# Performance work log

Hardware: AMD Instinct MI355X
Metric: run time of the kernel (lower is better)

## Reference

```python
import jax, jax.numpy as jnp
import numpy as np

B, N, C, H, REG = 1, 2309, 1024, 16, 5
D = C // H


def setup_inputs() -> dict:
    key = jax.random.key(0)
    k0, k1, k2, k3 = jax.random.split(key, 4)
    x = jax.random.normal(k0, (B, N, C), dtype=jnp.float32)
    g_info = jax.random.normal(k1, (12, 2, C), dtype=jnp.float32)
    W_qkv = jax.random.normal(k2, (C, 3 * C), dtype=jnp.float32) * 0.02
    W_proj = jax.random.normal(k3, (C, C), dtype=jnp.float32) * 0.02
    b_proj = jnp.zeros((C,), dtype=jnp.float32)
    return {"x": x, "g_info": g_info, "W_qkv": W_qkv, "W_proj": W_proj, "b_proj": b_proj}


def reference(x, g_info, W_qkv, W_proj, b_proj):
    Bx, Nx, Cx = x.shape
    scale = D ** -0.5
    # qkv projection (qkv_bias=False)
    qkv = (x @ W_qkv).reshape(Bx, Nx, 3, H, D)
    q, k, v = qkv[:, :, 0], qkv[:, :, 1], qkv[:, :, 2]  # [B,N,H,D]

    # grounding query vector from layer 0
    g_layer = g_info[0].reshape(-1, H, D)
    q_g = g_layer[0]  # [H,D]

    # cosine-similarity routing over non-register tokens
    q_pure = q[:, REG:]  # [B,M,H,D]
    q_n = q_pure / jnp.linalg.norm(q_pure, axis=-1, keepdims=True)
    qg_n = q_g / jnp.linalg.norm(q_g, axis=-1, keepdims=True)
    sim = (qg_n[None, None] * q_n).sum(-1).mean(-1)  # [B,M]
    sim = (sim - sim.min()) / (sim.max() - sim.min())  # global min-max normalize
    pos = sim > 0.9  # [B,M] boolean routing mask

    # Full logits computed once; group attention = masked softmax over the
    # group's key set (registers always included). This is mathematically
    # identical to the torch gather->attend->scatter, with static shapes.
    logits = jnp.einsum('bqhd,bkhd->bhqk', q * scale, k)  # [B,H,N,N]

    def masked_attn(tok_mask):
        key_mask = jnp.concatenate([jnp.ones((Bx, REG), bool), tok_mask], axis=1)  # [B,N]
        l = jnp.where(key_mask[:, None, None, :], logits, -jnp.inf)
        a = jax.nn.softmax(l, axis=-1)
        return jnp.einsum('bhqk,bkhd->bqhd', a, v)  # [B,N,H,D]

    x_pos = masked_attn(pos)
    x_neg = masked_attn(~pos)

    reg_out = (x_pos[:, :REG] + x_neg[:, :REG]) * 0.5
    tok_out = jnp.where(pos[:, :, None, None], x_pos[:, REG:], x_neg[:, REG:])
    out = jnp.concatenate([reg_out, tok_out], axis=1).reshape(Bx, Nx, Cx)
    return out @ W_proj + b_proj
```

## Files before the change

### kernel.cpp

```cpp
#include <hip/hip_runtime.h>
#include <math.h>

#define TOK 2309
#define CH 1024
#define NH 16
#define HD 64
#define NREG 5
#define NTOK (TOK - NREG)
#define NPADQ 2432
#define NPAD2 2560
#define NKT 40
#define HTILES 20
#define NQROW 2368
#define QSCL 0.1803368801f

typedef unsigned short ushort_t;
typedef unsigned char uchar_t;
typedef __attribute__((ext_vector_type(8))) short s8frag;
typedef __attribute__((ext_vector_type(4))) float f4frag;
typedef __attribute__((ext_vector_type(2))) long ll2;

__device__ __forceinline__ float wredsum(float v){
  #pragma unroll
  for (int o = 32; o > 0; o >>= 1) v += __shfl_xor(v, o, 64);
  return v;
}

__device__ __forceinline__ unsigned short f2bf(float x){
  union { float f; unsigned u; } v; v.f = x;
  unsigned r = v.u + 0x7FFF + ((v.u >> 16) & 1);
  return (unsigned short)(r >> 16);
}
__device__ __forceinline__ float bf2f(unsigned short u){
  union { unsigned u32; float f; } v; v.u32 = ((unsigned)u) << 16;
  return v.f;
}
__device__ __forceinline__ unsigned pack_bf16(float lo, float hi){
  union { float f; unsigned u; } a, b;
  a.f = lo; b.f = hi;
  return __builtin_amdgcn_perm(b.u + 0x8000u, a.u + 0x8000u, 0x07060302u);
}
__device__ __forceinline__ uchar_t f2fp8(float x){
  return (uchar_t)(__builtin_amdgcn_cvt_pk_fp8_f32(x, x, 0, false) & 0xff);
}
__device__ __forceinline__ void cp16(const void* g, void* l){
  __builtin_amdgcn_global_load_lds(
      (const __attribute__((address_space(1))) unsigned int*)g,
      (__attribute__((address_space(3))) unsigned int*)l, 16, 0, 0);
}

__global__ __launch_bounds__(256) void split_x_kernel(
    const float* __restrict__ X, ushort_t* __restrict__ Xhi, ushort_t* __restrict__ Xlo)
{
  int row = blockIdx.x;
  int c4 = threadIdx.x * 4;
  ushort4 h4 = {0,0,0,0}, l4 = {0,0,0,0};
  if (row < TOK) {
    float4 v = *(const float4*)&X[(size_t)row*CH + c4];
    float vv[4] = {v.x, v.y, v.z, v.w};
    ushort_t hs[4], ls[4];
    #pragma unroll
    for (int i = 0; i < 4; i++) {
      hs[i] = f2bf(vv[i]);
      ls[i] = f2bf(vv[i] - bf2f(hs[i]));
    }
    h4.x=hs[0]; h4.y=hs[1]; h4.z=hs[2]; h4.w=hs[3];
    l4.x=ls[0]; l4.y=ls[1]; l4.z=ls[2]; l4.w=ls[3];
  }
  *(ushort4*)&Xhi[(size_t)row*CH + c4] = h4;
  *(ushort4*)&Xlo[(size_t)row*CH + c4] = l4;
}

__global__ __launch_bounds__(256) void pack_w_kernel(
    const float* __restrict__ W, const int N,
    ushort_t* __restrict__ WT, ushort_t* __restrict__ WloT, const int loN)
{
  __shared__ float T[64][68];
  const int tid = threadIdx.x;
  const int n0 = blockIdx.x * 64;
  const int k0 = blockIdx.y * 64;
  const int lr = tid >> 4;
  const int lc = (tid & 15) * 4;
  #pragma unroll
  for (int s = 0; s < 4; s++) {
    float4 v = *(const float4*)&W[(size_t)(k0 + lr + s*16) * N + n0 + lc];
    *(float4*)&T[lr + s*16][lc] = v;
  }
  __syncthreads();
  const int nl = tid >> 2;
  const int kc = (tid & 3) * 16;
  const bool dolo = (WloT != nullptr) && (n0 < loN);
  ushort_t* dh = WT + (size_t)(n0 + nl) * CH + k0 + kc;
  ushort_t* dl = WloT + (size_t)(n0 + nl) * CH + k0 + kc;
  #pragma unroll
  for (int g = 0; g < 4; g++) {
    float a = T[kc+g*4+0][nl], b = T[kc+g*4+1][nl];
    float c = T[kc+g*4+2][nl], d = T[kc+g*4+3][nl];
    ushort4 oh;
    oh.x=f2bf(a); oh.y=f2bf(b); oh.z=f2bf(c); oh.w=f2bf(d);
    *(ushort4*)&dh[g*4] = oh;
    if (dolo) {
      ushort4 ol;
      ol.x=f2bf(a-bf2f(oh.x)); ol.y=f2bf(b-bf2f(oh.y));
      ol.z=f2bf(c-bf2f(oh.z)); ol.w=f2bf(d-bf2f(oh.w));
      *(ushort4*)&dl[g*4] = ol;
    }
  }
}

__global__ __launch_bounds__(256) void gemm_qkv_mfma(
    const ushort_t* __restrict__ Xhi, const ushort_t* __restrict__ Xlo,
    const ushort_t* __restrict__ WhiT, const ushort_t* __restrict__ WloT,
    float* __restrict__ Qf, uchar_t* __restrict__ Q8,
    uchar_t* __restrict__ K8, ushort_t* __restrict__ Vbf)
{
  __shared__ ushort_t LA[2][2][4096];
  __shared__ ushort_t LB[2][2][4096];
  const int tid = threadIdx.x;
  const int w = tid >> 6, lane = tid & 63;
  const int quad = lane >> 4, c16 = lane & 15;
  const int wm = w >> 1, wn = w & 1;
  const int nt = blockIdx.x, mt = blockIdx.y;
  const int n0 = nt * 128, m0 = mt * 128;
  const bool isQ = (nt < 8);

  const int srow = tid >> 2;
  const int g = (tid & 3) ^ ((tid >> 3) & 3);
  const size_t aoff = (size_t)(m0 + srow)*CH + g*8;
  const size_t boff = (size_t)(n0 + srow)*CH + g*8;
  const int lbase = (tid & 192) * 8;

  f4frag acc[4][4];
  #pragma unroll
  for (int mi = 0; mi < 4; mi++)
    #pragma unroll
    for (int nb = 0; nb < 4; nb++) acc[mi][nb] = (f4frag){0.f,0.f,0.f,0.f};

  const int soff = (quad ^ ((c16 >> 1) & 3)) * 8;
  int aro[4], bro[4];
  #pragma unroll
  for (int i = 0; i < 4; i++) {
    aro[i] = (wm*64 + i*16 + c16)*32 + soff;
    bro[i] = (wn*64 + i*16 + c16)*32 + soff;
  }

#define QKV_STAGE(KT, BUF) {                                                   \
    const int _k = (KT)*32;                                                    \
    cp16(Xhi  + aoff + _k,                 &LA[BUF][0][lbase]);                \
    cp16(Xhi  + aoff + _k + (size_t)64*CH, &LA[BUF][0][2048 + lbase]);         \
    cp16(WhiT + boff + _k,                 &LB[BUF][0][lbase]);                \
    cp16(WhiT + boff + _k + (size_t)64*CH, &LB[BUF][0][2048 + lbase]);         \
    if (isQ) {                                                                 \
      cp16(Xlo  + aoff + _k,                 &LA[BUF][1][lbase]);              \
      cp16(Xlo  + aoff + _k + (size_t)64*CH, &LA[BUF][1][2048 + lbase]);       \
      cp16(WloT + boff + _k,                 &LB[BUF][1][lbase]);              \
      cp16(WloT + boff + _k + (size_t)64*CH, &LB[BUF][1][2048 + lbase]);       \
    } }

  QKV_STAGE(0, 0);
  for (int kt = 0; kt < 32; kt++) {
    const int buf = kt & 1;
    __syncthreads();
    if (kt < 31) { QKV_STAGE(kt+1, buf^1); }
    s8frag a[4], b[4];
    #pragma unroll
    for (int i = 0; i < 4; i++) a[i] = *(const s8frag*)&LA[buf][0][aro[i]];
    #pragma unroll
    for (int i = 0; i < 4; i++) b[i] = *(const s8frag*)&LB[buf][0][bro[i]];
    #pragma unroll
    for (int mi = 0; mi < 4; mi++)
      #pragma unroll
      for (int nb = 0; nb < 4; nb++)
        acc[mi][nb] = __builtin_amdgcn_mfma_f32_16x16x32_bf16(a[mi], b[nb], acc[mi][nb], 0, 0, 0);
    if (isQ) {
      s8frag al[4], bl[4];
      #pragma unroll
      for (int i = 0; i < 4; i++) al[i] = *(const s8frag*)&LA[buf][1][aro[i]];
      #pragma unroll
      for (int i = 0; i < 4; i++) bl[i] = *(const s8frag*)&LB[buf][1][bro[i]];
      #pragma unroll
      for (int mi = 0; mi < 4; mi++)
        #pragma unroll
        for (int nb = 0; nb < 4; nb++) {
          acc[mi][nb] = __builtin_amdgcn_mfma_f32_16x16x32_bf16(a[mi],  bl[nb], acc[mi][nb], 0, 0, 0);
          acc[mi][nb] = __builtin_amdgcn_mfma_f32_16x16x32_bf16(al[mi], b[nb],  acc[mi][nb], 0, 0, 0);
        }
    }
  }
#undef QKV_STAGE

  const int three = (nt >= 16) ? 2 : (nt >= 8) ? 1 : 0;
  #pragma unroll
  for (int mi = 0; mi < 4; mi++) {
    const int orow = m0 + wm*64 + mi*16 + quad*4;
    if (three == 0) {
      #pragma unroll
      for (int nb = 0; nb < 4; nb++) {
        const int col = n0 + wn*64 + nb*16 + c16;
        const int h = (col >> 6) & 15, d = col & 63;
        float* qf = Qf + (size_t)h*TOK*HD;
        uchar_t* q8 = Q8 + (size_t)h*NPADQ*64;
        #pragma unroll
        for (int r = 0; r < 4; r++) {
          int row = orow + r;
          float v = (row < TOK) ? acc[mi][nb][r] : 0.f;
          if (row < TOK) qf[(size_t)row*HD + d] = v;
          q8[(size_t)row*64 + d] = f2fp8(v);
        }
      }
    } else if (three == 1) {
      #pragma unroll
      for (int nb = 0; nb < 4; nb++) {
        const int col = n0 + wn*64 + nb*16 + c16;
        const int h = (col >> 6) & 15;
        const int quadK = ((nb & 1) * 2) + (c16 >> 3);
        const int byteoff = (nb >> 1) * 8 + (c16 & 7);
        uchar_t* base = K8 + (size_t)h*NKT*4096;
        #pragma unroll
        for (int r = 0; r < 4; r++) {
          int row = orow + r;
          float v = (row < TOK) ? acc[mi][nb][r] : 0.f;
          int tile = row >> 6, b = (row >> 4) & 3, c16K = row & 15;
          base[(size_t)tile*4096 + b*1024 + (quadK*16 + c16K)*16 + byteoff] = f2fp8(v);
        }
      }
    } else {
      const int tile  = orow >> 6;
      const int vhalf = (orow >> 5) & 1;
      const int quadV = (orow >> 3) & 3;
      const int b0    = (orow & 7) * 2;
      #pragma unroll
      for (int nb = 0; nb < 4; nb++) {
        const int col = n0 + wn*64 + nb*16 + c16;
        const int h = (col >> 6) & 15;
        const int nbv = (col >> 4) & 3, c16V = col & 15;
        ushort_t* base = Vbf + (size_t)h*NKT*4096;
        ushort4 o;
        o.x = f2bf((orow+0 < TOK) ? acc[mi][nb][0] : 0.f);
        o.y = f2bf((orow+1 < TOK) ? acc[mi][nb][1] : 0.f);
        o.z = f2bf((orow+2 < TOK) ? acc[mi][nb][2] : 0.f);
        o.w = f2bf((orow+3 < TOK) ? acc[mi][nb][3] : 0.f);
        *(ushort4*)&base[(size_t)tile*4096 + nbv*1024 + vhalf*512
                         + (quadV*16 + c16V)*8 + (b0 >> 1)] = o;
      }
    }
  }
}

__global__ __launch_bounds__(256) void sim_kernel(
    const float* __restrict__ Q, const float* __restrict__ G, float* __restrict__ sim)
{
  const int tid = threadIdx.x;
  const int w = tid >> 6, lane = tid & 63;
  float qgn[NH];
  #pragma unroll
  for (int h = 0; h < NH; h++) {
    float g = G[h*HD + lane];
    float n2 = wredsum(g*g);
    qgn[h] = g / sqrtf(n2);
  }
  int it = blockIdx.x * 4 + w;
  if (it >= NTOK) return;
  int i = NREG + it;
  float acc = 0.f;
  #pragma unroll
  for (int h = 0; h < NH; h++) {
    float qv = Q[((size_t)h*TOK + i)*HD + lane];
    float dot = wredsum(qv * qgn[h]);
    float n2  = wredsum(qv * qv);
    acc += dot / sqrtf(n2);
  }
  if (lane == 0) sim[it] = acc * (1.0f/16.0f);
}

__global__ __launch_bounds__(256) void mask_kernel(
    const float* __restrict__ sim, int* __restrict__ cls,
    float* __restrict__ WP, float* __restrict__ WN)
{
  __shared__ float smn[256], smx[256];
  const int tid = threadIdx.x;
  float mn = 1e30f, mx = -1e30f;
  for (int i = tid; i < NTOK; i += 256) { float s = sim[i]; mn = fminf(mn, s); mx = fmaxf(mx, s); }
  smn[tid] = mn; smx[tid] = mx;
  __syncthreads();
  for (int off = 128; off > 0; off >>= 1) {
    if (tid < off) { smn[tid] = fminf(smn[tid], smn[tid+off]); smx[tid] = fmaxf(smx[tid], smx[tid+off]); }
    __syncthreads();
  }
  mn = smn[0]; mx = smx[0];
  float inv = 1.0f / (mx - mn);
  for (int j = tid; j < NPAD2; j += 256) {
    float wp = 0.f, wn = 0.f; int c = 0;
    if (j < NREG) { wp = 1.f; wn = 1.f; c = 2; }
    else if (j < TOK) {
      bool pos = ((sim[j-NREG] - mn) * inv) > 0.9f;
      c = pos ? 1 : 0;
      wp = pos ? 1.f : 0.f;
      wn = pos ? 0.f : 1.f;
    }
    WP[j] = wp; WN[j] = wn;
    if (j < TOK) cls[j] = c;
  }
}

__global__ __launch_bounds__(256) void attn_kernel(
    const uchar_t* __restrict__ Q8, const uchar_t* __restrict__ K8,
    const ushort_t* __restrict__ Vbf,
    const float* __restrict__ WP, const float* __restrict__ WN,
    ushort_t* __restrict__ POp, ushort_t* __restrict__ POn,
    float* __restrict__ Lp, float* __restrict__ Ln)
{
  __shared__ __align__(16) uchar_t smem[40960];
  uchar_t* Kst = smem;
  uchar_t* Vst = smem + 8192;
  const int tid = threadIdx.x;
  const int w = tid >> 6, lane = tid & 63;
  const int quad = lane >> 4, c16 = lane & 15;
  uchar_t* Pw  = smem + 24576 + w*4096;
  const int h = blockIdx.y;
  const int half = blockIdx.z;
  const int q0 = blockIdx.x * 64;

  const uchar_t* Qh = Q8 + (size_t)h * NPADQ * 64;
  const uchar_t* gk = K8 + ((size_t)h*NKT + half*HTILES)*4096 + tid*16;
  const uchar_t* gv = (const uchar_t*)Vbf + ((size_t)h*NKT + half*HTILES)*8192 + tid*16;
  const int lw = w * 1024;

  const uchar_t* qp = Qh + (size_t)(q0 + w*16 + c16)*64 + quad*8;
  const long qf0 = *(const long*)(qp);
  const long qf1 = *(const long*)(qp + 32);

  f4frag op[4], on[4];
  #pragma unroll
  for (int nb = 0; nb < 4; nb++) { op[nb] = (f4frag){0.f,0.f,0.f,0.f}; on[nb] = (f4frag){0.f,0.f,0.f,0.f}; }
  float lp = 0.f, ln = 0.f;

  cp16(gk, Kst + lw);
  cp16(gv, Vst + lw);
  cp16(gv + 4096, Vst + 4096 + lw);

  int pb = 0;
  for (int t = 0; t < HTILES; t++) {
    __syncthreads();
    if (t < HTILES-1) {
      cp16(gk + (size_t)(t+1)*4096, Kst + (pb^1)*4096 + lw);
      cp16(gv + (size_t)(t+1)*8192,        Vst + (pb^1)*8192 + lw);
      cp16(gv + (size_t)(t+1)*8192 + 4096, Vst + (pb^1)*8192 + 4096 + lw);
    }
    const int j0 = half*(HTILES*64) + t*64;
    f4frag st[4];
    #pragma unroll
    for (int b = 0; b < 4; b++) {
      ll2 kv = *(const ll2*)&Kst[pb*4096 + b*1024 + lane*16];
      f4frag z = (f4frag){0.f,0.f,0.f,0.f};
      z     = __builtin_amdgcn_mfma_f32_16x16x32_fp8_fp8(kv.x, qf0, z, 0, 0, 0);
      st[b] = __builtin_amdgcn_mfma_f32_16x16x32_fp8_fp8(kv.y, qf1, z, 0, 0, 0);
    }
    s8frag vf0[4], vf1[4];
    #pragma unroll
    for (int nb = 0; nb < 4; nb++) {
      vf0[nb] = *(const s8frag*)&Vst[pb*8192 + nb*2048 + lane*16];
      vf1[nb] = *(const s8frag*)&Vst[pb*8192 + nb*2048 + 1024 + lane*16];
    }
    #pragma unroll
    for (int b = 0; b < 4; b++) {
      float4 wp4 = *(const float4*)&WP[j0 + b*16 + quad*4];
      float4 wn4 = *(const float4*)&WN[j0 + b*16 + quad*4];
      float p0 = exp2f(st[b][0] * QSCL);
      float p1 = exp2f(st[b][1] * QSCL);
      float p2 = exp2f(st[b][2] * QSCL);
      float p3 = exp2f(st[b][3] * QSCL);
      float a0 = p0*wp4.x, a1 = p1*wp4.y, a2 = p2*wp4.z, a3 = p3*wp4.w;
      float b0 = p0*wn4.x, b1 = p1*wn4.y, b2 = p2*wn4.z, b3 = p3*wn4.w;
      lp += (a0+a1)+(a2+a3);
      ln += (b0+b1)+(b2+b3);
      uint2 pu, nu;
      pu.x = pack_bf16(a0, a1); pu.y = pack_bf16(a2, a3);
      nu.x = pack_bf16(b0, b1); nu.y = pack_bf16(b2, b3);
      const int chunk = b >> 1;
      const int quadA = (b & 1)*2 + (quad >> 1);
      const int addr = chunk*1024 + (quadA*16 + c16)*16 + (quad & 1)*8;
      *(uint2*)&Pw[addr]        = pu;
      *(uint2*)&Pw[2048 + addr] = nu;
    }
    s8frag ap0 = *(const s8frag*)&Pw[lane*16];
    s8frag ap1 = *(const s8frag*)&Pw[1024 + lane*16];
    s8frag an0 = *(const s8frag*)&Pw[2048 + lane*16];
    s8frag an1 = *(const s8frag*)&Pw[3072 + lane*16];
    #pragma unroll
    for (int nb = 0; nb < 4; nb++) {
      op[nb] = __builtin_amdgcn_mfma_f32_16x16x32_bf16(ap0, vf0[nb], op[nb], 0, 0, 0);
      op[nb] = __builtin_amdgcn_mfma_f32_16x16x32_bf16(ap1, vf1[nb], op[nb], 0, 0, 0);
      on[nb] = __builtin_amdgcn_mfma_f32_16x16x32_bf16(an0, vf0[nb], on[nb], 0, 0, 0);
      on[nb] = __builtin_amdgcn_mfma_f32_16x16x32_bf16(an1, vf1[nb], on[nb], 0, 0, 0);
    }
    pb ^= 1;
  }

  lp += __shfl_xor(lp, 16, 64); lp += __shfl_xor(lp, 32, 64);
  ln += __shfl_xor(ln, 16, 64); ln += __shfl_xor(ln, 32, 64);
  if (quad == 0) {
    int iq = q0 + w*16 + c16;
    if (iq < TOK) {
      Lp[((size_t)half*NH + h)*NQROW + iq] = lp;
      Ln[((size_t)half*NH + h)*NQROW + iq] = ln;
    }
  }
  __syncthreads();
  float* Sw = (float*)(smem + w*4608);
  const int q_l = lane >> 2;
  const int db  = (lane & 3) * 16;
  const int iq = q0 + w*16 + q_l;
  #pragma unroll
  for (int nb = 0; nb < 4; nb++)
    #pragma unroll
    for (int r = 0; r < 4; r++)
      Sw[(quad*4+r)*72 + nb*16+c16] = op[nb][r];
  float vp[16];
  #pragma unroll
  for (int i = 0; i < 16; i++) vp[i] = Sw[q_l*72 + db + i];
  #pragma unroll
  for (int nb = 0; nb < 4; nb++)
    #pragma unroll
    for (int r = 0; r < 4; r++)
      Sw[(quad*4+r)*72 + nb*16+c16] = on[nb][r];
  float vn[16];
  #pragma unroll
  for (int i = 0; i < 16; i++) vn[i] = Sw[q_l*72 + db + i];

  if (iq < TOK) {
    unsigned pk[8], nk[8];
    #pragma unroll
    for (int i = 0; i < 8; i++) {
      pk[i] = pack_bf16(vp[2*i], vp[2*i+1]);
      nk[i] = pack_bf16(vn[2*i], vn[2*i+1]);
    }
    size_t off = (size_t)half*NQROW*CH + (size_t)iq*CH + h*HD + db;
    *(uint4*)(POp + off)     = make_uint4(pk[0], pk[1], pk[2], pk[3]);
    *(uint4*)(POp + off + 8) = make_uint4(pk[4], pk[5], pk[6], pk[7]);
    *(uint4*)(POn + off)     = make_uint4(nk[0], nk[1], nk[2], nk[3]);
    *(uint4*)(POn + off + 8) = make_uint4(nk[4], nk[5], nk[6], nk[7]);
  }
}

__global__ __launch_bounds__(256) void merge_kernel(
    const ushort_t* __restrict__ POp, const ushort_t* __restrict__ POn,
    const float* __restrict__ Lp, const float* __restrict__ Ln,
    const int* __restrict__ cls, ushort_t* __restrict__ AObf)
{
  const int row = blockIdx.x;
  const int c4 = threadIdx.x * 4;
  const int h = c4 >> 6;
  const size_t o0 = (size_t)row*CH + c4;
  const size_t o1 = (size_t)NQROW*CH + o0;
  ushort4 p0 = *(const ushort4*)(POp + o0);
  ushort4 p1 = *(const ushort4*)(POp + o1);
  ushort4 n0 = *(const ushort4*)(POn + o0);
  ushort4 n1 = *(const ushort4*)(POn + o1);
  const float lpt = Lp[(size_t)h*NQROW + row] + Lp[(size_t)(NH+h)*NQROW + row];
  const float lnt = Ln[(size_t)h*NQROW + row] + Ln[(size_t)(NH+h)*NQROW + row];
  const float ilp = 1.f / lpt, iln = 1.f / lnt;
  const int cq = cls[row];
  float vp[4], vn[4], o[4];
  vp[0] = (bf2f(p0.x)+bf2f(p1.x))*ilp; vn[0] = (bf2f(n0.x)+bf2f(n1.x))*iln;
  vp[1] = (bf2f(p0.y)+bf2f(p1.y))*ilp; vn[1] = (bf2f(n0.y)+bf2f(n1.y))*iln;
  vp[2] = (bf2f(p0.z)+bf2f(p1.z))*ilp; vn[2] = (bf2f(n0.z)+bf2f(n1.z))*iln;
  vp[3] = (bf2f(p0.w)+bf2f(p1.w))*ilp; vn[3] = (bf2f(n0.w)+bf2f(n1.w))*iln;
  if (row < NREG) {
    #pragma unroll
    for (int i = 0; i < 4; i++) o[i] = 0.5f*(vp[i]+vn[i]);
  } else if (cq == 1) {
    #pragma unroll
    for (int i = 0; i < 4; i++) o[i] = vp[i];
  } else {
    #pragma unroll
    for (int i = 0; i < 4; i++) o[i] = vn[i];
  }
  uint2 pk;
  pk.x = pack_bf16(o[0], o[1]);
  pk.y = pack_bf16(o[2], o[3]);
  *(uint2*)(AObf + (size_t)row*CH + c4) = pk;
}

__global__ __launch_bounds__(256) void gemm_proj_mfma(
    const ushort_t* __restrict__ A, const ushort_t* __restrict__ WT,
    const float* __restrict__ bp, float* __restrict__ out)
{
  __shared__ ushort_t LA[2][4096];
  __shared__ ushort_t LB[2][4096];
  const int tid = threadIdx.x;
  const int w = tid >> 6, lane = tid & 63;
  const int quad = lane >> 4, c16 = lane & 15;
  const int wm = w >> 1, wn = w & 1;
  const int nt = blockIdx.x, mt = blockIdx.y;
  const int n0 = nt * 128, m0 = mt * 128;

  const int srow = tid >> 2;
  const int g = (tid & 3) ^ ((tid >> 3) & 3);
  const size_t aoff = (size_t)(m0 + srow)*CH + g*8;
  const size_t boff = (size_t)(n0 + srow)*CH + g*8;
  const int lbase = (tid & 192) * 8;

  f4frag acc[4][4];
  #pragma unroll
  for (int mi = 0; mi < 4; mi++)
    #pragma unroll
    for (int nb = 0; nb < 4; nb++) acc[mi][nb] = (f4frag){0.f,0.f,0.f,0.f};

  const int soff = (quad ^ ((c16 >> 1) & 3)) * 8;
  int aro[4], bro[4];
  #pragma unroll
  for (int i = 0; i < 4; i++) {
    aro[i] = (wm*64 + i*16 + c16)*32 + soff;
    bro[i] = (wn*64 + i*16 + c16)*32 + soff;
  }

#define PROJ_STAGE(KT, BUF) {                                                  \
    const int _k = (KT)*32;                                                    \
    cp16(A  + aoff + _k,                 &LA[BUF][lbase]);                     \
    cp16(A  + aoff + _k + (size_t)64*CH, &LA[BUF][2048 + lbase]);              \
    cp16(WT + boff + _k,                 &LB[BUF][lbase]);                     \
    cp16(WT + boff + _k + (size_t)64*CH, &LB[BUF][2048 + lbase]);              \
    }

  PROJ_STAGE(0, 0);
  for (int kt = 0; kt < 32; kt++) {
    const int buf = kt & 1;
    __syncthreads();
    if (kt < 31) { PROJ_STAGE(kt+1, buf^1); }
    s8frag a[4], b[4];
    #pragma unroll
    for (int i = 0; i < 4; i++) a[i] = *(const s8frag*)&LA[buf][aro[i]];
    #pragma unroll
    for (int i = 0; i < 4; i++) b[i] = *(const s8frag*)&LB[buf][bro[i]];
    #pragma unroll
    for (int mi = 0; mi < 4; mi++)
      #pragma unroll
      for (int nb = 0; nb < 4; nb++)
        acc[mi][nb] = __builtin_amdgcn_mfma_f32_16x16x32_bf16(a[mi], b[nb], acc[mi][nb], 0, 0, 0);
  }
#undef PROJ_STAGE

  #pragma unroll
  for (int mi = 0; mi < 4; mi++) {
    const int orow = m0 + wm*64 + mi*16 + quad*4;
    #pragma unroll
    for (int nb = 0; nb < 4; nb++) {
      const int col = n0 + wn*64 + nb*16 + c16;
      const float bias = bp[col];
      #pragma unroll
      for (int r = 0; r < 4; r++) {
        int row = orow + r;
        if (row < TOK) out[(size_t)row*CH + col] = acc[mi][nb][r] + bias;
      }
    }
  }
}

extern "C" void kernel_launch(void* const* d_in, const int* in_sizes, int n_in,
                              void* d_out, int out_size, void* d_ws, size_t ws_size,
                              hipStream_t stream) {
  const float* x      = (const float*)d_in[0];
  const float* g_info = (const float*)d_in[1];
  const float* W_qkv  = (const float*)d_in[2];
  const float* W_proj = (const float*)d_in[3];
  const float* b_proj = (const float*)d_in[4];
  float* out = (float*)d_out;

  float* ws = (float*)d_ws;
  float* Qf  = ws;
  float* SIM = Qf + (size_t)NH*TOK*HD;
  float* WP  = SIM + NTOK;
  float* WN  = WP + NPAD2;
  int*   CLS = (int*)(WN + NPAD2);
  float* LpB = (float*)(CLS + 2312);
  float* LnB = LpB + (size_t)2*NH*NQROW;
  ushort_t* Xhi    = (ushort_t*)(LnB + (size_t)2*NH*NQROW);
  ushort_t* Xlo    = Xhi    + (size_t)NPADQ*CH;
  ushort_t* WqkvT  = Xlo    + (size_t)NPADQ*CH;
  ushort_t* WqkvLo = WqkvT  + (size_t)3*CH*CH;
  ushort_t* WprojT = WqkvLo + (size_t)CH*CH;
  ushort_t* AObf   = WprojT + (size_t)CH*CH;
  ushort_t* POp    = AObf   + (size_t)NPADQ*CH;
  ushort_t* POn    = POp    + (size_t)2*NQROW*CH;
  uchar_t*  Q8     = (uchar_t*)(POn + (size_t)2*NQROW*CH);
  uchar_t*  K8     = Q8 + (size_t)NH*NPADQ*64;
  ushort_t* Vbf    = (ushort_t*)(K8 + (size_t)NH*NKT*4096);

  hipMemsetAsync(K8, 0, (size_t)NH*NKT*4096 + (size_t)NH*NKT*8192, stream);

  split_x_kernel<<<dim3(NPADQ), 256, 0, stream>>>(x, Xhi, Xlo);
  pack_w_kernel<<<dim3(48, 16), 256, 0, stream>>>(W_qkv, 3*CH, WqkvT, WqkvLo, CH);
  pack_w_kernel<<<dim3(16, 16), 256, 0, stream>>>(W_proj, CH, WprojT, nullptr, 0);
  gemm_qkv_mfma<<<dim3(24, 19), 256, 0, stream>>>(Xhi, Xlo, WqkvT, WqkvLo,
                                                  Qf, Q8, K8, Vbf);
  sim_kernel<<<dim3(576), 256, 0, stream>>>(Qf, g_info, SIM);
  mask_kernel<<<dim3(1), 256, 0, stream>>>(SIM, CLS, WP, WN);
  attn_kernel<<<dim3(37, NH, 2), 256, 0, stream>>>(Q8, K8, Vbf, WP, WN,
                                                   POp, POn, LpB, LnB);
  merge_kernel<<<dim3(TOK), 256, 0, stream>>>(POp, POn, LpB, LnB, CLS, AObf);
  gemm_proj_mfma<<<dim3(8, 19), 256, 0, stream>>>(AObf, WprojT, b_proj, out);
}
```

Before: 281.5 us.

## Compute transposed PV product in registers, drop P smem staging, shrink proj tiles

Reorders the V tile layout written by the QKV GEMM so the PV MFMA can take V as the A operand and the packed probabilities straight from registers as the B operand. This removes the per-wave shared-memory round trip for P and the smem transpose in the epilogue, and cuts attention LDS use from 40 KB to 24 KB so more blocks can be resident. It also switches to the hardware exp2 builtin, and halves the output-projection N tile to 64 to launch twice as many blocks. The risks are that the new V layout and transposed output indexing must match exactly, and the smaller projection tile reuses each loaded A tile less.

Result: faster. 257.1 us (-8.7%).

```diff
diff --git a/kernel.cpp b/kernel.cpp
--- a/kernel.cpp
+++ b/kernel.cpp
@@ -226,22 +226,23 @@
       }
     } else {
       const int tile  = orow >> 6;
-      const int vhalf = (orow >> 5) & 1;
-      const int quadV = (orow >> 3) & 3;
-      const int b0    = (orow & 7) * 2;
+      const int jj    = orow & 63;
+      const int c     = jj >> 5;
+      const int t16   = (jj >> 4) & 1;
+      const int quadA = (jj >> 2) & 3;
       #pragma unroll
       for (int nb = 0; nb < 4; nb++) {
         const int col = n0 + wn*64 + nb*16 + c16;
-        const int h = (col >> 6) & 15;
-        const int nbv = (col >> 4) & 3, c16V = col & 15;
+        const int h = (col >> 6) & 15, d = col & 63;
+        const int dblk = d >> 4, c16A = d & 15;
         ushort_t* base = Vbf + (size_t)h*NKT*4096;
         ushort4 o;
         o.x = f2bf((orow+0 < TOK) ? acc[mi][nb][0] : 0.f);
         o.y = f2bf((orow+1 < TOK) ? acc[mi][nb][1] : 0.f);
         o.z = f2bf((orow+2 < TOK) ? acc[mi][nb][2] : 0.f);
         o.w = f2bf((orow+3 < TOK) ? acc[mi][nb][3] : 0.f);
-        *(ushort4*)&base[(size_t)tile*4096 + nbv*1024 + vhalf*512
-                         + (quadV*16 + c16V)*8 + (b0 >> 1)] = o;
+        *(ushort4*)&base[(size_t)tile*4096 + dblk*1024 + c*512
+                         + (quadA*16 + c16A)*8 + 4*t16] = o;
       }
     }
   }
@@ -310,13 +311,12 @@
     ushort_t* __restrict__ POp, ushort_t* __restrict__ POn,
     float* __restrict__ Lp, float* __restrict__ Ln)
 {
-  __shared__ __align__(16) uchar_t smem[40960];
+  __shared__ __align__(16) uchar_t smem[24576];
   uchar_t* Kst = smem;
   uchar_t* Vst = smem + 8192;
   const int tid = threadIdx.x;
   const int w = tid >> 6, lane = tid & 63;
   const int quad = lane >> 4, c16 = lane & 15;
-  uchar_t* Pw  = smem + 24576 + w*4096;
   const int h = blockIdx.y;
   const int half = blockIdx.z;
   const int q0 = blockIdx.x * 64;
@@ -356,90 +356,59 @@
       z     = __builtin_amdgcn_mfma_f32_16x16x32_fp8_fp8(kv.x, qf0, z, 0, 0, 0);
       st[b] = __builtin_amdgcn_mfma_f32_16x16x32_fp8_fp8(kv.y, qf1, z, 0, 0, 0);
     }
-    s8frag vf0[4], vf1[4];
-    #pragma unroll
-    for (int nb = 0; nb < 4; nb++) {
-      vf0[nb] = *(const s8frag*)&Vst[pb*8192 + nb*2048 + lane*16];
-      vf1[nb] = *(const s8frag*)&Vst[pb*8192 + nb*2048 + 1024 + lane*16];
-    }
+    unsigned pu[4][2], nu[4][2];
     #pragma unroll
     for (int b = 0; b < 4; b++) {
       float4 wp4 = *(const float4*)&WP[j0 + b*16 + quad*4];
       float4 wn4 = *(const float4*)&WN[j0 + b*16 + quad*4];
-      float p0 = exp2f(st[b][0] * QSCL);
-      float p1 = exp2f(st[b][1] * QSCL);
-      float p2 = exp2f(st[b][2] * QSCL);
-      float p3 = exp2f(st[b][3] * QSCL);
+      float p0 = __builtin_amdgcn_exp2f(st[b][0] * QSCL);
+      float p1 = __builtin_amdgcn_exp2f(st[b][1] * QSCL);
+      float p2 = __builtin_amdgcn_exp2f(st[b][2] * QSCL);
+      float p3 = __builtin_amdgcn_exp2f(st[b][3] * QSCL);
       float a0 = p0*wp4.x, a1 = p1*wp4.y, a2 = p2*wp4.z, a3 = p3*wp4.w;
       float b0 = p0*wn4.x, b1 = p1*wn4.y, b2 = p2*wn4.z, b3 = p3*wn4.w;
       lp += (a0+a1)+(a2+a3);
       ln += (b0+b1)+(b2+b3);
-      uint2 pu, nu;
-      pu.x = pack_bf16(a0, a1); pu.y = pack_bf16(a2, a3);
-      nu.x = pack_bf16(b0, b1); nu.y = pack_bf16(b2, b3);
-      const int chunk = b >> 1;
-      const int quadA = (b & 1)*2 + (quad >> 1);
-      const int addr = chunk*1024 + (quadA*16 + c16)*16 + (quad & 1)*8;
-      *(uint2*)&Pw[addr]        = pu;
-      *(uint2*)&Pw[2048 + addr] = nu;
-    }
-    s8frag ap0 = *(const s8frag*)&Pw[lane*16];
-    s8frag ap1 = *(const s8frag*)&Pw[1024 + lane*16];
-    s8frag an0 = *(const s8frag*)&Pw[2048 + lane*16];
-    s8frag an1 = *(const s8frag*)&Pw[3072 + lane*16];
+      pu[b][0] = pack_bf16(a0, a1); pu[b][1] = pack_bf16(a2, a3);
+      nu[b][0] = pack_bf16(b0, b1); nu[b][1] = pack_bf16(b2, b3);
+    }
+    union Frag { unsigned u[4]; s8frag v; };
+    Frag fp0, fp1, fn0, fn1;
+    fp0.u[0]=pu[0][0]; fp0.u[1]=pu[0][1]; fp0.u[2]=pu[1][0]; fp0.u[3]=pu[1][1];
+    fp1.u[0]=pu[2][0]; fp1.u[1]=pu[2][1]; fp1.u[2]=pu[3][0]; fp1.u[3]=pu[3][1];
+    fn0.u[0]=nu[0][0]; fn0.u[1]=nu[0][1]; fn0.u[2]=nu[1][0]; fn0.u[3]=nu[1][1];
+    fn1.u[0]=nu[2][0]; fn1.u[1]=nu[2][1]; fn1.u[2]=nu[3][0]; fn1.u[3]=nu[3][1];
     #pragma unroll
     for (int nb = 0; nb < 4; nb++) {
-      op[nb] = __builtin_amdgcn_mfma_f32_16x16x32_bf16(ap0, vf0[nb], op[nb], 0, 0, 0);
-      op[nb] = __builtin_amdgcn_mfma_f32_16x16x32_bf16(ap1, vf1[nb], op[nb], 0, 0, 0);
-      on[nb] = __builtin_amdgcn_mfma_f32_16x16x32_bf16(an0, vf0[nb], on[nb], 0, 0, 0);
-      on[nb] = __builtin_amdgcn_mfma_f32_16x16x32_bf16(an1, vf1[nb], on[nb], 0, 0, 0);
+      s8frag va = *(const s8frag*)&Vst[pb*8192 + nb*2048 + lane*16];
+      s8frag vb = *(const s8frag*)&Vst[pb*8192 + nb*2048 + 1024 + lane*16];
+      op[nb] = __builtin_amdgcn_mfma_f32_16x16x32_bf16(va, fp0.v, op[nb], 0, 0, 0);
+      op[nb] = __builtin_amdgcn_mfma_f32_16x16x32_bf16(vb, fp1.v, op[nb], 0, 0, 0);
+      on[nb] = __builtin_amdgcn_mfma_f32_16x16x32_bf16(va, fn0.v, on[nb], 0, 0, 0);
+      on[nb] = __builtin_amdgcn_mfma_f32_16x16x32_bf16(vb, fn1.v, on[nb], 0, 0, 0);
     }
     pb ^= 1;
   }
 
   lp += __shfl_xor(lp, 16, 64); lp += __shfl_xor(lp, 32, 64);
   ln += __shfl_xor(ln, 16, 64); ln += __shfl_xor(ln, 32, 64);
-  if (quad == 0) {
-    int iq = q0 + w*16 + c16;
-    if (iq < TOK) {
-      Lp[((size_t)half*NH + h)*NQROW + iq] = lp;
-      Ln[((size_t)half*NH + h)*NQROW + iq] = ln;
-    }
-  }
-  __syncthreads();
-  float* Sw = (float*)(smem + w*4608);
-  const int q_l = lane >> 2;
-  const int db  = (lane & 3) * 16;
-  const int iq = q0 + w*16 + q_l;
-  #pragma unroll
-  for (int nb = 0; nb < 4; nb++)
-    #pragma unroll
-    for (int r = 0; r < 4; r++)
-      Sw[(quad*4+r)*72 + nb*16+c16] = op[nb][r];
-  float vp[16];
-  #pragma unroll
-  for (int i = 0; i < 16; i++) vp[i] = Sw[q_l*72 + db + i];
-  #pragma unroll
-  for (int nb = 0; nb < 4; nb++)
-    #pragma unroll
-    for (int r = 0; r < 4; r++)
-      Sw[(quad*4+r)*72 + nb*16+c16] = on[nb][r];
-  float vn[16];
-  #pragma unroll
-  for (int i = 0; i < 16; i++) vn[i] = Sw[q_l*72 + db + i];
-
+  const int iq = q0 + w*16 + c16;
+  if (quad == 0 && iq < TOK) {
+    Lp[((size_t)half*NH + h)*NQROW + iq] = lp;
+    Ln[((size_t)half*NH + h)*NQROW + iq] = ln;
+  }
   if (iq < TOK) {
-    unsigned pk[8], nk[8];
-    #pragma unroll
-    for (int i = 0; i < 8; i++) {
-      pk[i] = pack_bf16(vp[2*i], vp[2*i+1]);
-      nk[i] = pack_bf16(vn[2*i], vn[2*i+1]);
-    }
-    size_t off = (size_t)half*NQROW*CH + (size_t)iq*CH + h*HD + db;
-    *(uint4*)(POp + off)     = make_uint4(pk[0], pk[1], pk[2], pk[3]);
-    *(uint4*)(POp + off + 8) = make_uint4(pk[4], pk[5], pk[6], pk[7]);
-    *(uint4*)(POn + off)     = make_uint4(nk[0], nk[1], nk[2], nk[3]);
-    *(uint4*)(POn + off + 8) = make_uint4(nk[4], nk[5], nk[6], nk[7]);
+    const size_t base = (size_t)half*NQROW*CH + (size_t)iq*CH + h*HD;
+    #pragma unroll
+    for (int nb = 0; nb < 4; nb++) {
+      uint2 po, no;
+      po.x = pack_bf16(op[nb][0], op[nb][1]);
+      po.y = pack_bf16(op[nb][2], op[nb][3]);
+      no.x = pack_bf16(on[nb][0], on[nb][1]);
+      no.y = pack_bf16(on[nb][2], on[nb][3]);
+      *(uint2*)(POp + base + nb*16 + quad*4) = po;
+      *(uint2*)(POn + base + nb*16 + quad*4) = no;
+    }
   }
 }
 
@@ -487,13 +456,13 @@
     const float* __restrict__ bp, float* __restrict__ out)
 {
   __shared__ ushort_t LA[2][4096];
-  __shared__ ushort_t LB[2][4096];
+  __shared__ ushort_t LB[2][2048];
   const int tid = threadIdx.x;
   const int w = tid >> 6, lane = tid & 63;
   const int quad = lane >> 4, c16 = lane & 15;
   const int wm = w >> 1, wn = w & 1;
   const int nt = blockIdx.x, mt = blockIdx.y;
-  const int n0 = nt * 128, m0 = mt * 128;
+  const int n0 = nt * 64, m0 = mt * 128;
 
   const int srow = tid >> 2;
   const int g = (tid & 3) ^ ((tid >> 3) & 3);
@@ -501,26 +470,24 @@
   const size_t boff = (size_t)(n0 + srow)*CH + g*8;
   const int lbase = (tid & 192) * 8;
 
-  f4frag acc[4][4];
+  f4frag acc[4][2];
   #pragma unroll
   for (int mi = 0; mi < 4; mi++)
     #pragma unroll
-    for (int nb = 0; nb < 4; nb++) acc[mi][nb] = (f4frag){0.f,0.f,0.f,0.f};
+    for (int nb = 0; nb < 2; nb++) acc[mi][nb] = (f4frag){0.f,0.f,0.f,0.f};
 
   const int soff = (quad ^ ((c16 >> 1) & 3)) * 8;
-  int aro[4], bro[4];
-  #pragma unroll
-  for (int i = 0; i < 4; i++) {
-    aro[i] = (wm*64 + i*16 + c16)*32 + soff;
-    bro[i] = (wn*64 + i*16 + c16)*32 + soff;
-  }
+  int aro[4], bro[2];
+  #pragma unroll
+  for (int i = 0; i < 4; i++) aro[i] = (wm*64 + i*16 + c16)*32 + soff;
+  #pragma unroll
+  for (int i = 0; i < 2; i++) bro[i] = (wn*32 + i*16 + c16)*32 + soff;
 
 #define PROJ_STAGE(KT, BUF) {                                                  \
     const int _k = (KT)*32;                                                    \
     cp16(A  + aoff + _k,                 &LA[BUF][lbase]);                     \
     cp16(A  + aoff + _k + (size_t)64*CH, &LA[BUF][2048 + lbase]);              \
     cp16(WT + boff + _k,                 &LB[BUF][lbase]);                     \
-    cp16(WT + boff + _k + (size_t)64*CH, &LB[BUF][2048 + lbase]);              \
     }
 
   PROJ_STAGE(0, 0);
@@ -528,15 +495,15 @@
     const int buf = kt & 1;
     __syncthreads();
     if (kt < 31) { PROJ_STAGE(kt+1, buf^1); }
-    s8frag a[4], b[4];
+    s8frag a[4], b[2];
     #pragma unroll
     for (int i = 0; i < 4; i++) a[i] = *(const s8frag*)&LA[buf][aro[i]];
     #pragma unroll
-    for (int i = 0; i < 4; i++) b[i] = *(const s8frag*)&LB[buf][bro[i]];
+    for (int i = 0; i < 2; i++) b[i] = *(const s8frag*)&LB[buf][bro[i]];
     #pragma unroll
     for (int mi = 0; mi < 4; mi++)
       #pragma unroll
-      for (int nb = 0; nb < 4; nb++)
+      for (int nb = 0; nb < 2; nb++)
         acc[mi][nb] = __builtin_amdgcn_mfma_f32_16x16x32_bf16(a[mi], b[nb], acc[mi][nb], 0, 0, 0);
   }
 #undef PROJ_STAGE
@@ -545,8 +512,8 @@
   for (int mi = 0; mi < 4; mi++) {
     const int orow = m0 + wm*64 + mi*16 + quad*4;
     #pragma unroll
-    for (int nb = 0; nb < 4; nb++) {
-      const int col = n0 + wn*64 + nb*16 + c16;
+    for (int nb = 0; nb < 2; nb++) {
+      const int col = n0 + wn*32 + nb*16 + c16;
       const float bias = bp[col];
       #pragma unroll
       for (int r = 0; r < 4; r++) {
@@ -599,5 +566,5 @@
   attn_kernel<<<dim3(37, NH, 2), 256, 0, stream>>>(Q8, K8, Vbf, WP, WN,
                                                    POp, POn, LpB, LnB);
   merge_kernel<<<dim3(TOK), 256, 0, stream>>>(POp, POn, LpB, LnB, CLS, AObf);
-  gemm_proj_mfma<<<dim3(8, 19), 256, 0, stream>>>(AObf, WprojT, b_proj, out);
-}
+  gemm_proj_mfma<<<dim3(16, 19), 256, 0, stream>>>(AObf, WprojT, b_proj, out);
+}
```
